# Performance work log

Hardware: AMD Instinct MI355X
Metric: run time of the kernel (lower is better)

## Reference

```python
import jax, jax.numpy as jnp
import numpy as np

B = 131072

def _grid_P():
    # P[k] = ((i-6)/6, (j-6)/6, 1) with k = 13*i + j
    ii, jj = jnp.meshgrid(jnp.arange(13), jnp.arange(13), indexing='ij')
    P = jnp.stack([(ii - 6) / 6.0, (jj - 6) / 6.0, jnp.ones_like(ii)], axis=-1)
    return P.reshape(169, 3).astype(jnp.float32)  # [169,3], shared across batch

def setup_inputs() -> dict:
    key = jax.random.key(0)
    k0, k1, k2, k3, k4 = jax.random.split(key, 5)
    return {
        'eyes': jax.random.normal(k0, (B, 3), dtype=jnp.float32),
        'v': jax.random.normal(k1, (B, 3), dtype=jnp.float32),
        'R': jax.random.normal(k2, (B, 3, 3), dtype=jnp.float32),
        't': jax.random.normal(k3, (B, 3), dtype=jnp.float32),
        'alpha': jax.random.uniform(k4, (B,), dtype=jnp.float32),
    }

def reference(eyes, v, R, t, alpha):
    P = _grid_P()  # [169,3]
    # normalize gaze direction (clamped L2 norm, as in torch)
    vn = v / jnp.clip(jnp.linalg.norm(v, axis=1, keepdims=True), 1e-14, None)
    # M = v v^T - alpha * I   [B,3,3]
    M = vn[:, :, None] * vn[:, None, :] - alpha[:, None, None] * jnp.eye(3, dtype=v.dtype)
    # rows of the projection basis: v1 = R[:,:,0], v2 = R[:,:,1], t - eyes
    W = jnp.stack([R[:, :, 0], R[:, :, 1], t - eyes], axis=1)  # [B,3,3]
    # sigma[b,a,c] = W[b,a,:] @ M[b] @ W[b,c,:]
    sigma = jnp.einsum('bai,bij,bcj->bac', W, M, W)  # [B,3,3]
    # quadratic form per grid point: out[b,k] = P[k] @ sigma[b] @ P[k]
    out = jnp.einsum('ki,bij,kj->bk', P, sigma, P)  # [B,169]
    return out
```

## Files before the change

kernel.cpp:

```cpp
#include <hip/hip_runtime.h>

#define NB   6
#define NOUT (NB * 169)
#define BLK  256

__global__ __launch_bounds__(BLK) void ConeProjection_68642167325009_kernel(
    const float* __restrict__ eyes,
    const float* __restrict__ v,
    const float* __restrict__ R,
    const float* __restrict__ t,
    const float* __restrict__ alpha,
    float* __restrict__ out,
    int B)
{
    __shared__ float c[NB][6];
    const int tid = threadIdx.x;
    const int b0  = blockIdx.x * NB;

    if (tid < NB) {
        const int b = b0 + tid;
        if (b < B) {
            float vx = v[b*3+0], vy = v[b*3+1], vz = v[b*3+2];
            float n  = sqrtf(vx*vx + vy*vy + vz*vz);
            n = fmaxf(n, 1e-14f);
            const float inv = 1.0f / n;
            vx *= inv; vy *= inv; vz *= inv;
            const float a = alpha[b];

            const float* Rb = R + (size_t)b * 9;
            const float w0x = Rb[0], w0y = Rb[3], w0z = Rb[6];
            const float w1x = Rb[1], w1y = Rb[4], w1z = Rb[7];
            const float w2x = t[b*3+0] - eyes[b*3+0];
            const float w2y = t[b*3+1] - eyes[b*3+1];
            const float w2z = t[b*3+2] - eyes[b*3+2];

            const float d0 = vx*w0x + vy*w0y + vz*w0z;
            const float d1 = vx*w1x + vy*w1y + vz*w1z;
            const float d2 = vx*w2x + vy*w2y + vz*w2z;

            const float s00 = d0*d0 - a*(w0x*w0x + w0y*w0y + w0z*w0z);
            const float s11 = d1*d1 - a*(w1x*w1x + w1y*w1y + w1z*w1z);
            const float s22 = d2*d2 - a*(w2x*w2x + w2y*w2y + w2z*w2z);
            const float s01 = d0*d1 - a*(w0x*w1x + w0y*w1y + w0z*w1z);
            const float s02 = d0*d2 - a*(w0x*w2x + w0y*w2y + w0z*w2z);
            const float s12 = d1*d2 - a*(w1x*w2x + w1y*w2y + w1z*w2z);

            c[tid][0] = s00;
            c[tid][1] = s11;
            c[tid][2] = s22;
            c[tid][3] = 2.0f * s01;
            c[tid][4] = 2.0f * s02;
            c[tid][5] = 2.0f * s12;
        }
    }
    __syncthreads();

    const size_t base = (size_t)blockIdx.x * NOUT;
    #pragma unroll
    for (int r = 0; r < 4; ++r) {
        const int local = tid + r * BLK;
        if (local < NOUT) {
            const int bl = (local * 388) >> 16;
            const int k  = local - 169 * bl;
            if (b0 + bl < B) {
                const int i = (k * 20165) >> 18;
                const int j = k - 13 * i;
                const float px = (float)(i - 6) * (1.0f / 6.0f);
                const float py = (float)(j - 6) * (1.0f / 6.0f);
                const float val = c[bl][2]
                                + px * (c[bl][0] * px + c[bl][3] * py + c[bl][4])
                                + py * (c[bl][1] * py + c[bl][5]);
                out[base + local] = val;
            }
        }
    }
}

extern "C" void kernel_launch(void* const* d_in, const int* in_sizes, int n_in,
                              void* d_out, int out_size, void* d_ws, size_t ws_size,
                              hipStream_t stream) {
    const float* eyes  = (const float*)d_in[0];
    const float* v     = (const float*)d_in[1];
    const float* R     = (const float*)d_in[2];
    const float* t     = (const float*)d_in[3];
    const float* alpha = (const float*)d_in[4];
    float* out = (float*)d_out;

    const int B = in_sizes[4];
    const int grid = (B + NB - 1) / NB;

    ConeProjection_68642167325009_kernel<<<grid, BLK, 0, stream>>>(
        eyes, v, R, t, alpha, out, B);
}
```

Before: 117.2 us.

## Split into coefficient kernel and vectorized float4 grid-stride output kernel

Computes the six quadratic-form coefficients per batch in a first kernel with all threads active and stores them to workspace. A second grid-stride kernel then writes the output as float4 stores, working out batch and grid indices per element. The aim is to drop the single-wave, serialized coefficient phase and the syncthreads inside each block, and to widen the output stores. In exchange it adds a second launch and a workspace round trip, and it assumes the output length is divisible by 4.

```diff
diff --git a/kernel.cpp b/kernel.cpp
--- a/kernel.cpp
+++ b/kernel.cpp
@@ -1,78 +1,83 @@
 #include <hip/hip_runtime.h>
 
-#define NB   6
-#define NOUT (NB * 169)
-#define BLK  256
+#define BLK 256
 
-__global__ __launch_bounds__(BLK) void ConeProjection_68642167325009_kernel(
+__global__ __launch_bounds__(BLK) void cone_coeff_kernel(
     const float* __restrict__ eyes,
     const float* __restrict__ v,
     const float* __restrict__ R,
     const float* __restrict__ t,
     const float* __restrict__ alpha,
-    float* __restrict__ out,
+    float* __restrict__ c,
     int B)
 {
-    __shared__ float c[NB][6];
-    const int tid = threadIdx.x;
-    const int b0  = blockIdx.x * NB;
+    const int b = blockIdx.x * BLK + threadIdx.x;
+    if (b >= B) return;
 
-    if (tid < NB) {
-        const int b = b0 + tid;
-        if (b < B) {
-            float vx = v[b*3+0], vy = v[b*3+1], vz = v[b*3+2];
-            float n  = sqrtf(vx*vx + vy*vy + vz*vz);
-            n = fmaxf(n, 1e-14f);
-            const float inv = 1.0f / n;
-            vx *= inv; vy *= inv; vz *= inv;
-            const float a = alpha[b];
+    float vx = v[b*3+0], vy = v[b*3+1], vz = v[b*3+2];
+    float n  = sqrtf(vx*vx + vy*vy + vz*vz);
+    n = fmaxf(n, 1e-14f);
+    const float inv = 1.0f / n;
+    vx *= inv; vy *= inv; vz *= inv;
+    const float a = alpha[b];
 
-            const float* Rb = R + (size_t)b * 9;
-            const float w0x = Rb[0], w0y = Rb[3], w0z = Rb[6];
-            const float w1x = Rb[1], w1y = Rb[4], w1z = Rb[7];
-            const float w2x = t[b*3+0] - eyes[b*3+0];
-            const float w2y = t[b*3+1] - eyes[b*3+1];
-            const float w2z = t[b*3+2] - eyes[b*3+2];
+    const float* Rb = R + (size_t)b * 9;
+    const float w0x = Rb[0], w0y = Rb[3], w0z = Rb[6];
+    const float w1x = Rb[1], w1y = Rb[4], w1z = Rb[7];
+    const float w2x = t[b*3+0] - eyes[b*3+0];
+    const float w2y = t[b*3+1] - eyes[b*3+1];
+    const float w2z = t[b*3+2] - eyes[b*3+2];
 
-            const float d0 = vx*w0x + vy*w0y + vz*w0z;
-            const float d1 = vx*w1x + vy*w1y + vz*w1z;
-            const float d2 = vx*w2x + vy*w2y + vz*w2z;
+    const float d0 = vx*w0x + vy*w0y + vz*w0z;
+    const float d1 = vx*w1x + vy*w1y + vz*w1z;
+    const float d2 = vx*w2x + vy*w2y + vz*w2z;
 
-            const float s00 = d0*d0 - a*(w0x*w0x + w0y*w0y + w0z*w0z);
-            const float s11 = d1*d1 - a*(w1x*w1x + w1y*w1y + w1z*w1z);
-            const float s22 = d2*d2 - a*(w2x*w2x + w2y*w2y + w2z*w2z);
-            const float s01 = d0*d1 - a*(w0x*w1x + w0y*w1y + w0z*w1z);
-            const float s02 = d0*d2 - a*(w0x*w2x + w0y*w2y + w0z*w2z);
-            const float s12 = d1*d2 - a*(w1x*w2x + w1y*w2y + w1z*w2z);
+    const float s00 = d0*d0 - a*(w0x*w0x + w0y*w0y + w0z*w0z);
+    const float s11 = d1*d1 - a*(w1x*w1x + w1y*w1y + w1z*w1z);
+    const float s22 = d2*d2 - a*(w2x*w2x + w2y*w2y + w2z*w2z);
+    const float s01 = d0*d1 - a*(w0x*w1x + w0y*w1y + w0z*w1z);
+    const float s02 = d0*d2 - a*(w0x*w2x + w0y*w2y + w0z*w2z);
+    const float s12 = d1*d2 - a*(w1x*w2x + w1y*w2y + w1z*w2z);
 
-            c[tid][0] = s00;
-            c[tid][1] = s11;
-            c[tid][2] = s22;
-            c[tid][3] = 2.0f * s01;
-            c[tid][4] = 2.0f * s02;
-            c[tid][5] = 2.0f * s12;
+    float4* c4 = (float4*)c;
+    c4[2*b+0] = make_float4(s00, s11, s22, 2.0f*s01);
+    c4[2*b+1] = make_float4(2.0f*s02, 2.0f*s12, 0.0f, 0.0f);
+}
+
+__global__ __launch_bounds__(BLK) void cone_write_kernel(
+    const float* __restrict__ c,
+    float* __restrict__ out,
+    int total4)
+{
+    const int stride = gridDim.x * BLK;
+    const float4* __restrict__ c4 = (const float4*)c;
+    float4* __restrict__ out4 = (float4*)out;
+
+    for (int i = blockIdx.x * BLK + threadIdx.x; i < total4; i += stride) {
+        const int n0 = i * 4;
+        int b = (int)(((unsigned long long)n0 * 1626496491ULL) >> 38);
+        int k = n0 - 169 * b;
+
+        float4 lo = c4[2*b+0];
+        float4 hi = c4[2*b+1];
+
+        float r[4];
+        #pragma unroll
+        for (int e = 0; e < 4; ++e) {
+            if (k == 169) {
+                ++b; k = 0;
+                lo = c4[2*b+0];
+                hi = c4[2*b+1];
+            }
+            const int iq = (k * 20165) >> 18;
+            const int j  = k - 13 * iq;
+            const float px = (float)(iq - 6) * (1.0f / 6.0f);
+            const float py = (float)(j  - 6) * (1.0f / 6.0f);
+            r[e] = lo.z + px * (lo.x * px + lo.w * py + hi.x)
+                        + py * (lo.y * py + hi.y);
+            ++k;
         }
-    }
-    __syncthreads();
-
-    const size_t base = (size_t)blockIdx.x * NOUT;
-    #pragma unroll
-    for (int r = 0; r < 4; ++r) {
-        const int local = tid + r * BLK;
-        if (local < NOUT) {
-            const int bl = (local * 388) >> 16;
-            const int k  = local - 169 * bl;
-            if (b0 + bl < B) {
-                const int i = (k * 20165) >> 18;
-                const int j = k - 13 * i;
-                const float px = (float)(i - 6) * (1.0f / 6.0f);
-                const float py = (float)(j - 6) * (1.0f / 6.0f);
-                const float val = c[bl][2]
-                                + px * (c[bl][0] * px + c[bl][3] * py + c[bl][4])
-                                + py * (c[bl][1] * py + c[bl][5]);
-                out[base + local] = val;
-            }
-        }
+        out4[i] = make_float4(r[0], r[1], r[2], r[3]);
     }
 }
 
@@ -85,10 +90,14 @@
     const float* t     = (const float*)d_in[3];
     const float* alpha = (const float*)d_in[4];
     float* out = (float*)d_out;
+    float* c   = (float*)d_ws;
 
     const int B = in_sizes[4];
-    const int grid = (B + NB - 1) / NB;
+    const int total4 = out_size / 4;
 
-    ConeProjection_68642167325009_kernel<<<grid, BLK, 0, stream>>>(
-        eyes, v, R, t, alpha, out, B);
+    const int grid1 = (B + BLK - 1) / BLK;
+    cone_coeff_kernel<<<grid1, BLK, 0, stream>>>(eyes, v, R, t, alpha, c, B);
+
+    const int grid2 = 4096;
+    cone_write_kernel<<<grid2, BLK, 0, stream>>>(c, out, total4);
 }
```

After: 112.2 us. 1.04x faster.
